# Performance work log

Measured on AMD Instinct MI355X. Metric: run time of the kernel, lower is better.

## Reference

```python
import math
import jax, jax.numpy as jnp
import numpy as np

B, T, D, H, L, DFF = 8, 256, 256, 8, 4, 1024
RBF_DIM = 128
TIME_DIM = D - RBF_DIM  # 128
VOCAB = 64
DH = D // H
RBF_GAP = 0.05
CENTERS = jnp.linspace(0.0, 6.4, RBF_DIM)


def _ln(x, g, b, eps=1e-6):
    m = jnp.mean(x, -1, keepdims=True)
    v = jnp.mean((x - m) ** 2, -1, keepdims=True)
    return (x - m) * jax.lax.rsqrt(v + eps) * g + b


def setup_inputs() -> dict:
    key = jax.random.key(0)
    ks = jax.random.split(key, 24)
    s = 0.02

    def W(k, *shape):
        return jax.random.normal(k, shape, jnp.float32) * s

    emb = W(ks[0], VOCAB, D).at[0].set(0.0)  # padding_idx=0
    return {
        'src': jax.random.randint(ks[1], (B, T), 0, VOCAB),
        'lengths': jax.random.randint(ks[2], (B,), T // 2, T + 1),
        'bond_matrix': jax.random.uniform(ks[3], (B, T, T), jnp.float32, 0.0, 6.4),
        'timestep': jax.random.uniform(ks[4], (B,), jnp.float32, 0.0, 1000.0),
        'emb_table': emb,
        't_w1': W(ks[5], TIME_DIM, TIME_DIM), 't_b1': jnp.zeros((TIME_DIM,), jnp.float32),
        't_w2': W(ks[6], TIME_DIM, TIME_DIM), 't_b2': jnp.zeros((TIME_DIM,), jnp.float32),
        'u': jax.random.normal(ks[7], (D,), jnp.float32) * s,
        'v': jax.random.normal(ks[8], (D,), jnp.float32) * s,
        'Wq': W(ks[9], L, D, D), 'bq': jnp.zeros((L, D), jnp.float32),
        'Wk': W(ks[10], L, D, D), 'bk': jnp.zeros((L, D), jnp.float32),
        'Wv': W(ks[11], L, D, D), 'bv': jnp.zeros((L, D), jnp.float32),
        'Wo': W(ks[12], L, D, D), 'bo': jnp.zeros((L, D), jnp.float32),
        'ln1_g': jnp.ones((L, D), jnp.float32), 'ln1_b': jnp.zeros((L, D), jnp.float32),
        'ln2_g': jnp.ones((L, D), jnp.float32), 'ln2_b': jnp.zeros((L, D), jnp.float32),
        'ff_w1': W(ks[13], L, D, DFF), 'ff_b1': jnp.zeros((L, DFF), jnp.float32),
        'ff_w2': W(ks[14], L, DFF, D), 'ff_b2': jnp.zeros((L, D), jnp.float32),
        'lnf_g': jnp.ones((D,), jnp.float32), 'lnf_b': jnp.zeros((D,), jnp.float32),
    }


def _forward(src, lengths, bond_matrix, timestep, emb_table, t_w1, t_b1, t_w2, t_b2,
             u, v, Wq, bq, Wk, bk, Wv, bv, Wo, bo, ln1_g, ln1_b, ln2_g, ln2_b,
             ff_w1, ff_b1, ff_w2, ff_b2, lnf_g, lnf_b):
    pad = jnp.arange(T) >= lengths[:, None]            # [B,T] True = padding
    pair_mask = pad[:, None, :] | pad[:, :, None]      # [B,T,T]
    # RBF expansion of distances; padded pairs pushed to 1e9 -> rbf ~ 0
    dmat = jnp.where(pair_mask, 1e9, bond_matrix)
    rbf = jnp.exp(-(dmat[..., None] - CENTERS) ** 2 / RBF_GAP)   # [B,T,T,RBF_DIM]
    # sinusoidal timestep embedding -> MLP (Linear, SiLU, Linear)
    half = TIME_DIM // 2
    freqs = jnp.exp(-jnp.log(jnp.asarray(10000.0, jnp.float32)) * jnp.arange(half, dtype=jnp.float32) / half)
    ang = timestep[:, None] * freqs
    temb = jnp.concatenate([jnp.cos(ang), jnp.sin(ang)], -1)
    temb = jax.nn.silu(temb @ t_w1 + t_b1) @ t_w2 + t_b2          # [B,TIME_DIM]
    # pairwise relative embedding: concat(rbf, broadcast time) -> [B,T,T,D]
    rel = jnp.concatenate([rbf, jnp.broadcast_to(temb[:, None, None, :], (B, T, T, TIME_DIM))], -1)
    rel = rel.reshape(B, T, T, H, DH)

    x = emb_table[src]                                  # [B,T,D]
    amask = pad[:, None, None, :]                       # [B,1,1,T]
    uu = u.reshape(H, 1, DH)
    vv = v.reshape(H, 1, DH)
    scale = 1.0 / math.sqrt(DH)

    def step(x, p):
        wq, bq_, wk, bk_, wv, bv_, wo, bo_, g1, b1_, g2, b2_, w1, fb1, w2, fb2 = p
        h = _ln(x, g1, b1_)
        q = (h @ wq + bq_).reshape(B, T, H, DH).transpose(0, 2, 1, 3) * scale
        k = (h @ wk + bk_).reshape(B, T, H, DH).transpose(0, 2, 1, 3)
        val = (h @ wv + bv_).reshape(B, T, H, DH).transpose(0, 2, 1, 3)
        a_c = jnp.einsum('bhqd,bhkd->bhqk', q + uu, k)            # content score
        b_d = jnp.einsum('bhqd,bqkhd->bhqk', q + vv, rel)         # relative-position score
        scores = jnp.where(amask, -1e18, a_c + b_d)
        attn = jax.nn.softmax(scores, -1)
        ctx = jnp.einsum('bhqk,bhkd->bqhd', attn, val).reshape(B, T, D)
        out = ctx @ wo + bo_ + x
        h2 = _ln(out, g2, b2_)
        return jax.nn.relu(h2 @ w1 + fb1) @ w2 + fb2 + out, None

    x, _ = jax.lax.scan(step, x, (Wq, bq, Wk, bk, Wv, bv, Wo, bo,
                                  ln1_g, ln1_b, ln2_g, ln2_b,
                                  ff_w1, ff_b1, ff_w2, ff_b2))
    return _ln(x, lnf_g, lnf_b)


def reference(src, lengths, bond_matrix, timestep, emb_table, t_w1, t_b1, t_w2, t_b2,
              u, v, Wq, bq, Wk, bk, Wv, bv, Wo, bo, ln1_g, ln1_b, ln2_g, ln2_b,
              ff_w1, ff_b1, ff_w2, ff_b2, lnf_g, lnf_b):
    return _forward(src, lengths, bond_matrix, timestep, emb_table, t_w1, t_b1, t_w2, t_b2,
                    u, v, Wq, bq, Wk, bk, Wv, bv, Wo, bo, ln1_g, ln1_b, ln2_g, ln2_b,
                    ff_w1, ff_b1, ff_w2, ff_b2, lnf_g, lnf_b)
```

## Files before the change

kernel.cpp:

```cpp
#include <hip/hip_runtime.h>
#include <hip/hip_bf16.h>
#include <math.h>

#define BB 8
#define TT 256
#define DD 256
#define HH 8
#define DHH 32
#define LL 4
#define DFF 1024
#define QTILE 16

#define RBF_DELTA 0.05039370078740158f
#define RBF_INVGAP 20.0f

typedef __attribute__((ext_vector_type(8))) short short8v;
typedef __attribute__((ext_vector_type(4))) short short4v;
typedef __attribute__((ext_vector_type(4))) float f32x4;

__device__ __forceinline__ ushort f2bf(float x) {
    __hip_bfloat16 h = __float2bfloat16(x);
    return *reinterpret_cast<ushort*>(&h);
}

__global__ void transpose_bf16_kernel(const float* __restrict__ in, ushort* __restrict__ out,
                                      int K, int N, int lstride) {
    __shared__ float tile[32][33];
    int l = blockIdx.z;
    const float* W = in + (size_t)l * lstride;
    ushort* Wt = out + (size_t)l * lstride;
    int kb = blockIdx.y * 32, nb = blockIdx.x * 32;
    int tx = threadIdx.x, ty = threadIdx.y;
#pragma unroll
    for (int i = 0; i < 4; i++) {
        int r = ty + i * 8;
        tile[r][tx] = W[(kb + r) * N + nb + tx];
    }
    __syncthreads();
#pragma unroll
    for (int i = 0; i < 4; i++) {
        int r = ty + i * 8;
        Wt[(nb + r) * K + kb + tx] = f2bf(tile[tx][r]);
    }
}

__global__ void temb_kernel(const float* __restrict__ timestep,
                            const float* __restrict__ t_w1, const float* __restrict__ t_b1,
                            const float* __restrict__ t_w2, const float* __restrict__ t_b2,
                            float* __restrict__ temb_out) {
    __shared__ float s0[128], s1[128];
    int b = blockIdx.x, j = threadIdx.x;
    float ts = timestep[b];
    const float LOG1E4 = 9.210340371976184f;
    if (j < 64) {
        float f = expf(-LOG1E4 * (float)j / 64.f);
        s0[j] = cosf(ts * f);
    } else {
        int i = j - 64;
        float f = expf(-LOG1E4 * (float)i / 64.f);
        s0[j] = sinf(ts * f);
    }
    __syncthreads();
    float acc = t_b1[j];
    for (int i = 0; i < 128; i++) acc += s0[i] * t_w1[i * 128 + j];
    acc = acc / (1.f + expf(-acc));
    s1[j] = acc;
    __syncthreads();
    float acc2 = t_b2[j];
    for (int i = 0; i < 128; i++) acc2 += s1[i] * t_w2[i * 128 + j];
    temb_out[b * 128 + j] = acc2;
}

__global__ void embed_kernel(const int* __restrict__ src, const float* __restrict__ emb,
                             float* __restrict__ x) {
    int r = blockIdx.x, d = threadIdx.x;
    x[r * DD + d] = emb[src[r] * DD + d];
}

template <int OUT_BF16>
__global__ void ln_kernel(const float* __restrict__ in, const float* __restrict__ g,
                          const float* __restrict__ bta, void* __restrict__ out) {
    __shared__ float red[8];
    __shared__ float mv[2];
    int r = blockIdx.x, t = threadIdx.x;
    float v = in[r * DD + t];
    float s = v, s2 = v * v;
    for (int off = 32; off > 0; off >>= 1) {
        s += __shfl_xor(s, off);
        s2 += __shfl_xor(s2, off);
    }
    int w = t >> 6;
    if ((t & 63) == 0) { red[w] = s; red[4 + w] = s2; }
    __syncthreads();
    if (t == 0) {
        float S = red[0] + red[1] + red[2] + red[3];
        float S2 = red[4] + red[5] + red[6] + red[7];
        float m = S * (1.f / 256.f);
        float var = S2 * (1.f / 256.f) - m * m;
        mv[0] = m; mv[1] = rsqrtf(var + 1e-6f);
    }
    __syncthreads();
    float o = (v - mv[0]) * mv[1] * g[t] + bta[t];
    if (OUT_BF16) ((ushort*)out)[r * DD + t] = f2bf(o);
    else          ((float*)out)[r * DD + t] = o;
}

__device__ __forceinline__ void gemm_mfma_body(
    const ushort* __restrict__ A, const ushort* __restrict__ Wt,
    const float* __restrict__ bias, const float* __restrict__ resid,
    void* __restrict__ out, int N, int K, float scale, int RELU, int OUT_BF16) {
    __shared__ __align__(16) ushort smem[10240];
    ushort* As = smem;
    ushort* Bs = smem + 2048;
    float* red = (float*)smem;

    int tid = threadIdx.x;
    int w = tid >> 6, lane = tid & 63;
    int m0 = blockIdx.y * 16, n0 = blockIdx.x * 64;

    f32x4 acc[4] = {f32x4{0,0,0,0}, f32x4{0,0,0,0}, f32x4{0,0,0,0}, f32x4{0,0,0,0}};

    for (int k0 = 0; k0 < K; k0 += 128) {
        {
            int r = tid >> 4, k8 = tid & 15;
            short8v av = *reinterpret_cast<const short8v*>(&A[(m0 + r) * K + k0 + k8 * 8]);
            int dstb = r * 256 + ((k8 * 16) ^ ((r & 7) << 4));
            *reinterpret_cast<short8v*>((char*)As + dstb) = av;
        }
#pragma unroll
        for (int it = 0; it < 4; it++) {
            int idx = it * 256 + tid;
            int r = idx >> 4, k8 = idx & 15;
            short8v bv = *reinterpret_cast<const short8v*>(&Wt[(n0 + r) * K + k0 + k8 * 8]);
            int dstb = r * 256 + ((k8 * 16) ^ ((r & 7) << 4));
            *reinterpret_cast<short8v*>((char*)Bs + dstb) = bv;
        }
        __syncthreads();
        int kb = w * 64 + (lane >> 4) * 16;
        int arow = lane & 15;
        short8v a = *reinterpret_cast<const short8v*>(
            (char*)As + arow * 256 + (kb ^ ((arow & 7) << 4)));
#pragma unroll
        for (int nb = 0; nb < 4; nb++) {
            int nrow = nb * 16 + (lane & 15);
            short8v b = *reinterpret_cast<const short8v*>(
                (char*)Bs + nrow * 256 + (kb ^ ((nrow & 7) << 4)));
            acc[nb] = __builtin_amdgcn_mfma_f32_16x16x32_bf16(a, b, acc[nb], 0, 0, 0);
        }
        __syncthreads();
    }
    if (w > 0) {
        float* r0 = &red[((w - 1) * 64 + lane) * 16];
#pragma unroll
        for (int nb = 0; nb < 4; nb++)
            *reinterpret_cast<f32x4*>(&r0[nb * 4]) = acc[nb];
    }
    __syncthreads();
    if (w == 0) {
        const float* r0 = &red[lane * 16];
        const float* r1 = &red[(64 + lane) * 16];
        const float* r2 = &red[(128 + lane) * 16];
        int col = lane & 15;
#pragma unroll
        for (int nb = 0; nb < 4; nb++) {
            int n = n0 + nb * 16 + col;
            float bia = bias[n];
#pragma unroll
            for (int i = 0; i < 4; i++) {
                int idx = nb * 4 + i;
                int m = m0 + (lane >> 4) * 4 + i;
                float v = acc[nb][i] + r0[idx] + r1[idx] + r2[idx];
                v = (v + bia) * scale;
                if (RELU) v = fmaxf(v, 0.f);
                if (resid) v += resid[m * N + n];
                if (OUT_BF16) ((ushort*)out)[m * N + n] = f2bf(v);
                else          ((float*)out)[m * N + n] = v;
            }
        }
    }
}

template <int RELU, int OUT_BF16>
__global__ __launch_bounds__(256) void gemm_bf16(
    const ushort* __restrict__ A, const ushort* __restrict__ Wt,
    const float* __restrict__ bias, const float* __restrict__ resid,
    void* __restrict__ out, int N, int K, float scale) {
    gemm_mfma_body(A, Wt, bias, resid, out, N, K, scale, RELU, OUT_BF16);
}

__global__ __launch_bounds__(256) void qkv_bf16(
    const ushort* __restrict__ A,
    const ushort* __restrict__ Wqt, const float* __restrict__ bq, float* __restrict__ qo,
    const ushort* __restrict__ Wkt, const float* __restrict__ bk, float* __restrict__ ko,
    const ushort* __restrict__ Wvt, const float* __restrict__ bv, float* __restrict__ vo,
    float qscale) {
    int z = blockIdx.z;
    const ushort* W = (z == 0) ? Wqt : (z == 1) ? Wkt : Wvt;
    const float* bi = (z == 0) ? bq : (z == 1) ? bk : bv;
    float* o = (z == 0) ? qo : (z == 1) ? ko : vo;
    float sc = (z == 0) ? qscale : 1.f;
    gemm_mfma_body(A, W, bi, nullptr, o, DD, DD, sc, 0, 0);
}

__global__ __launch_bounds__(256, 2) void attn_kernel(
    const float* __restrict__ qbuf, const float* __restrict__ kbuf,
    const float* __restrict__ vbuf, const float* __restrict__ u,
    const float* __restrict__ v, const float* __restrict__ temb,
    const float* __restrict__ bond, const int* __restrict__ lengths,
    ushort* __restrict__ ctx) {
    __shared__ float KV[256][33];
    __shared__ float sc[QTILE][257];
    __shared__ float qu_s[QTILE][32], qv_s[QTILE][32];
    __shared__ float tq[QTILE];
    __shared__ float temb_s[32];

    int qt = blockIdx.x;
    int h  = blockIdx.y;
    int b  = blockIdx.z;
    int t  = threadIdx.x;
    int len = lengths[b];
    int q0 = qt * QTILE;

    for (int e = t; e < QTILE * 32; e += 256) {
        int q = e >> 5, dh = e & 31;
        float qs = qbuf[(b * TT + q0 + q) * DD + h * 32 + dh];
        qu_s[q][dh] = qs + u[h * 32 + dh];
        qv_s[q][dh] = qs + v[h * 32 + dh];
    }
    if (t < 32) temb_s[t] = (h >= 4) ? temb[b * 128 + (h - 4) * 32 + t] : 0.f;
    for (int e = t; e < 256 * 32; e += 256) {
        int k = e >> 5, dh = e & 31;
        KV[k][dh] = kbuf[(b * TT + k) * DD + h * 32 + dh];
    }
    __syncthreads();

    if (t < QTILE) {
        float a = 0.f;
#pragma unroll
        for (int j = 0; j < 32; j++) a += qv_s[t][j] * temb_s[j];
        tq[t] = a;
    }
    __syncthreads();

    {
        int k = t;
        bool kvalid = k < len;
        float c0 = (float)(h * 32) * RBF_DELTA;
        for (int q = 0; q < QTILE; q++) {
            float s;
            if (!kvalid) {
                s = -1e18f;
            } else {
                float accA = 0.f;
#pragma unroll
                for (int dh = 0; dh < 32; dh++) accA += qu_s[q][dh] * KV[k][dh];
                float accB;
                if (h < 4) {
                    accB = 0.f;
                    if (q0 + q < len) {
                        float d = bond[(b * TT + q0 + q) * TT + k];
#pragma unroll
                        for (int j = 0; j < 32; j++) {
                            float diff = d - (c0 + j * RBF_DELTA);
                            accB += qv_s[q][j] * __expf(-diff * diff * RBF_INVGAP);
                        }
                    }
                } else {
                    accB = tq[q];
                }
                s = accA + accB;
            }
            sc[q][k] = s;
        }
    }
    __syncthreads();

    {
        int r = t >> 4, j = t & 15;
        float vals[16];
        float mx = -1e30f;
#pragma unroll
        for (int i = 0; i < 16; i++) {
            vals[i] = sc[r][j + 16 * i];
            mx = fmaxf(mx, vals[i]);
        }
        for (int off = 8; off > 0; off >>= 1) mx = fmaxf(mx, __shfl_xor(mx, off));
        float sum = 0.f;
#pragma unroll
        for (int i = 0; i < 16; i++) {
            float e = __expf(vals[i] - mx);
            vals[i] = e; sum += e;
        }
        for (int off = 8; off > 0; off >>= 1) sum += __shfl_xor(sum, off);
        float inv = 1.f / sum;
#pragma unroll
        for (int i = 0; i < 16; i++) sc[r][j + 16 * i] = vals[i] * inv;
    }
    for (int e = t; e < 256 * 32; e += 256) {
        int k2 = e >> 5, dh = e & 31;
        KV[k2][dh] = vbuf[(b * TT + k2) * DD + h * 32 + dh];
    }
    __syncthreads();

    {
        int dh = t & 31, qq = t >> 5;
#pragma unroll
        for (int rep = 0; rep < 2; rep++) {
            int q = qq + 8 * rep;
            float acc = 0.f;
#pragma unroll 8
            for (int k2 = 0; k2 < 256; k2++) acc += sc[q][k2] * KV[k2][dh];
            ctx[(b * TT + q0 + q) * DD + h * 32 + dh] = f2bf(acc);
        }
    }
}

extern "C" void kernel_launch(void* const* d_in, const int* in_sizes, int n_in,
                              void* d_out, int out_size, void* d_ws, size_t ws_size,
                              hipStream_t stream) {
    const int*   src      = (const int*)  d_in[0];
    const int*   lengths  = (const int*)  d_in[1];
    const float* bond     = (const float*)d_in[2];
    const float* timestep = (const float*)d_in[3];
    const float* emb      = (const float*)d_in[4];
    const float* t_w1     = (const float*)d_in[5];
    const float* t_b1     = (const float*)d_in[6];
    const float* t_w2     = (const float*)d_in[7];
    const float* t_b2     = (const float*)d_in[8];
    const float* u        = (const float*)d_in[9];
    const float* v        = (const float*)d_in[10];
    const float* Wq       = (const float*)d_in[11];
    const float* bq       = (const float*)d_in[12];
    const float* Wk       = (const float*)d_in[13];
    const float* bk       = (const float*)d_in[14];
    const float* Wv       = (const float*)d_in[15];
    const float* bv       = (const float*)d_in[16];
    const float* Wo       = (const float*)d_in[17];
    const float* bo       = (const float*)d_in[18];
    const float* ln1_g    = (const float*)d_in[19];
    const float* ln1_b    = (const float*)d_in[20];
    const float* ln2_g    = (const float*)d_in[21];
    const float* ln2_b    = (const float*)d_in[22];
    const float* ff_w1    = (const float*)d_in[23];
    const float* ff_b1    = (const float*)d_in[24];
    const float* ff_w2    = (const float*)d_in[25];
    const float* ff_b2    = (const float*)d_in[26];
    const float* lnf_g    = (const float*)d_in[27];
    const float* lnf_b    = (const float*)d_in[28];

    float* ws   = (float*)d_ws;
    float* xbuf = ws;
    float* qbuf = xbuf + 524288;
    float* kbuf = qbuf + 524288;
    float* vbuf = kbuf + 524288;
    float* obuf = vbuf + 524288;
    float* temb = obuf + 524288;
    ushort* hbuf_bf  = (ushort*)(temb + 1024);
    ushort* cbuf_bf  = hbuf_bf + 524288;
    ushort* ffbuf_bf = cbuf_bf + 524288;
    ushort* wqt_bf   = ffbuf_bf + 2097152;
    ushort* wkt_bf   = wqt_bf + 262144;
    ushort* wvt_bf   = wkt_bf + 262144;
    ushort* wot_bf   = wvt_bf + 262144;
    ushort* ffw1t_bf = wot_bf + 262144;
    ushort* ffw2t_bf = ffw1t_bf + 1048576;

    dim3 tb(32, 8);
    transpose_bf16_kernel<<<dim3(8, 8, 4), tb, 0, stream>>>(Wq, wqt_bf, 256, 256, 65536);
    transpose_bf16_kernel<<<dim3(8, 8, 4), tb, 0, stream>>>(Wk, wkt_bf, 256, 256, 65536);
    transpose_bf16_kernel<<<dim3(8, 8, 4), tb, 0, stream>>>(Wv, wvt_bf, 256, 256, 65536);
    transpose_bf16_kernel<<<dim3(8, 8, 4), tb, 0, stream>>>(Wo, wot_bf, 256, 256, 65536);
    transpose_bf16_kernel<<<dim3(32, 8, 4), tb, 0, stream>>>(ff_w1, ffw1t_bf, 256, 1024, 262144);
    transpose_bf16_kernel<<<dim3(8, 32, 4), tb, 0, stream>>>(ff_w2, ffw2t_bf, 1024, 256, 262144);

    temb_kernel<<<8, 128, 0, stream>>>(timestep, t_w1, t_b1, t_w2, t_b2, temb);
    embed_kernel<<<2048, 256, 0, stream>>>(src, emb, xbuf);

    const float scale = 0.17677669529663687f;
    dim3 gqkv(4, 128, 3);
    dim3 g256(4, 128);
    dim3 g1024(16, 128);

    for (int l = 0; l < LL; l++) {
        ln_kernel<1><<<2048, 256, 0, stream>>>(xbuf, ln1_g + l * 256, ln1_b + l * 256, hbuf_bf);
        qkv_bf16<<<gqkv, 256, 0, stream>>>(hbuf_bf,
            wqt_bf + l * 65536, bq + l * 256, qbuf,
            wkt_bf + l * 65536, bk + l * 256, kbuf,
            wvt_bf + l * 65536, bv + l * 256, vbuf, scale);
        attn_kernel<<<dim3(16, 8, 8), 256, 0, stream>>>(qbuf, kbuf, vbuf, u, v, temb, bond, lengths, cbuf_bf);
        gemm_bf16<0, 0><<<g256, 256, 0, stream>>>(cbuf_bf, wot_bf + l * 65536, bo + l * 256, xbuf, obuf, 256, 256, 1.f);
        ln_kernel<1><<<2048, 256, 0, stream>>>(obuf, ln2_g + l * 256, ln2_b + l * 256, hbuf_bf);
        gemm_bf16<1, 1><<<g1024, 256, 0, stream>>>(hbuf_bf, ffw1t_bf + l * 262144, ff_b1 + l * 1024, nullptr, ffbuf_bf, 1024, 256, 1.f);
        gemm_bf16<0, 0><<<g256, 256, 0, stream>>>(ffbuf_bf, ffw2t_bf + l * 262144, ff_b2 + l * 256, obuf, xbuf, 256, 1024, 1.f);
    }
    ln_kernel<0><<<2048, 256, 0, stream>>>(xbuf, lnf_g, lnf_b, (float*)d_out);
}
```

Measured before the change: 606.2 us.

## Restructure attention kernel: swizzled K/V smem, K in registers, vectorized loads, exp2 RBF

Replaces the padded K/V shared-memory tiles with an XOR-swizzled layout and caches each thread's key row in registers, so the score loop reads q through broadcast float4 loads. The RBF term now uses exp2f with a prefolded constant and an incremental diff instead of recomputing each centre. The score row stride is padded to 260 so float4 reads of the score tile are aligned, and launch bounds request 3 blocks per CU. The cost is more register pressure from the 32-float key cache alongside a higher occupancy target, which could cause spills.

```diff
diff --git a/kernel.cpp b/kernel.cpp
--- a/kernel.cpp
+++ b/kernel.cpp
@@ -12,7 +12,7 @@
 #define QTILE 16
 
 #define RBF_DELTA 0.05039370078740158f
-#define RBF_INVGAP 20.0f
+#define RBF_NEGK -28.853900817779268f
 
 typedef __attribute__((ext_vector_type(8))) short short8v;
 typedef __attribute__((ext_vector_type(4))) short short4v;
@@ -202,14 +202,14 @@
     gemm_mfma_body(A, W, bi, nullptr, o, DD, DD, sc, 0, 0);
 }
 
-__global__ __launch_bounds__(256, 2) void attn_kernel(
+__global__ __launch_bounds__(256, 3) void attn_kernel(
     const float* __restrict__ qbuf, const float* __restrict__ kbuf,
     const float* __restrict__ vbuf, const float* __restrict__ u,
     const float* __restrict__ v, const float* __restrict__ temb,
     const float* __restrict__ bond, const int* __restrict__ lengths,
     ushort* __restrict__ ctx) {
-    __shared__ float KV[256][33];
-    __shared__ float sc[QTILE][257];
+    __shared__ float KV[256 * 32];
+    __shared__ float sc[QTILE][260];
     __shared__ float qu_s[QTILE][32], qv_s[QTILE][32];
     __shared__ float tq[QTILE];
     __shared__ float temb_s[32];
@@ -230,7 +230,7 @@
     if (t < 32) temb_s[t] = (h >= 4) ? temb[b * 128 + (h - 4) * 32 + t] : 0.f;
     for (int e = t; e < 256 * 32; e += 256) {
         int k = e >> 5, dh = e & 31;
-        KV[k][dh] = kbuf[(b * TT + k) * DD + h * 32 + dh];
+        KV[k * 32 + (dh ^ (k & 31))] = kbuf[(b * TT + k) * DD + h * 32 + dh];
     }
     __syncthreads();
 
@@ -241,6 +241,13 @@
         tq[t] = a;
     }
     __syncthreads();
+
+    float kreg[32];
+    {
+        int kx = t & 31;
+#pragma unroll
+        for (int dh = 0; dh < 32; dh++) kreg[dh] = KV[t * 32 + (dh ^ kx)];
+    }
 
     {
         int k = t;
@@ -251,18 +258,35 @@
             if (!kvalid) {
                 s = -1e18f;
             } else {
+                const float* qur = qu_s[q];
                 float accA = 0.f;
 #pragma unroll
-                for (int dh = 0; dh < 32; dh++) accA += qu_s[q][dh] * KV[k][dh];
+                for (int c = 0; c < 8; c++) {
+                    float4 q4 = *reinterpret_cast<const float4*>(&qur[c * 4]);
+                    accA = fmaf(q4.x, kreg[c * 4 + 0], accA);
+                    accA = fmaf(q4.y, kreg[c * 4 + 1], accA);
+                    accA = fmaf(q4.z, kreg[c * 4 + 2], accA);
+                    accA = fmaf(q4.w, kreg[c * 4 + 3], accA);
+                }
                 float accB;
                 if (h < 4) {
                     accB = 0.f;
                     if (q0 + q < len) {
-                        float d = bond[(b * TT + q0 + q) * TT + k];
-#pragma unroll
-                        for (int j = 0; j < 32; j++) {
-                            float diff = d - (c0 + j * RBF_DELTA);
-                            accB += qv_s[q][j] * __expf(-diff * diff * RBF_INVGAP);
+                        float d = bond[(size_t)(b * TT + q0 + q) * TT + k];
+                        float diff = d - c0;
+                        const float* qvr = qv_s[q];
+#pragma unroll
+                        for (int c = 0; c < 8; c++) {
+                            float4 q4 = *reinterpret_cast<const float4*>(&qvr[c * 4]);
+                            float p;
+                            p = exp2f(diff * diff * RBF_NEGK);
+                            accB = fmaf(q4.x, p, accB); diff -= RBF_DELTA;
+                            p = exp2f(diff * diff * RBF_NEGK);
+                            accB = fmaf(q4.y, p, accB); diff -= RBF_DELTA;
+                            p = exp2f(diff * diff * RBF_NEGK);
+                            accB = fmaf(q4.z, p, accB); diff -= RBF_DELTA;
+                            p = exp2f(diff * diff * RBF_NEGK);
+                            accB = fmaf(q4.w, p, accB); diff -= RBF_DELTA;
                         }
                     }
                 } else {
@@ -270,7 +294,7 @@
                 }
                 s = accA + accB;
             }
-            sc[q][k] = s;
+            sc[q][t] = s;
         }
     }
     __syncthreads();
@@ -298,7 +322,7 @@
     }
     for (int e = t; e < 256 * 32; e += 256) {
         int k2 = e >> 5, dh = e & 31;
-        KV[k2][dh] = vbuf[(b * TT + k2) * DD + h * 32 + dh];
+        KV[k2 * 32 + (dh ^ (k2 & 31))] = vbuf[(b * TT + k2) * DD + h * 32 + dh];
     }
     __syncthreads();
 
@@ -309,7 +333,13 @@
             int q = qq + 8 * rep;
             float acc = 0.f;
 #pragma unroll 8
-            for (int k2 = 0; k2 < 256; k2++) acc += sc[q][k2] * KV[k2][dh];
+            for (int kk = 0; kk < 256; kk += 4) {
+                float4 s4 = *reinterpret_cast<const float4*>(&sc[q][kk]);
+                acc = fmaf(s4.x, KV[(kk + 0) * 32 + (dh ^ ((kk + 0) & 31))], acc);
+                acc = fmaf(s4.y, KV[(kk + 1) * 32 + (dh ^ ((kk + 1) & 31))], acc);
+                acc = fmaf(s4.z, KV[(kk + 2) * 32 + (dh ^ ((kk + 2) & 31))], acc);
+                acc = fmaf(s4.w, KV[(kk + 3) * 32 + (dh ^ ((kk + 3) & 31))], acc);
+            }
             ctx[(b * TT + q0 + q) * DD + h * 32 + dh] = f2bf(acc);
         }
     }
```

Measured after the change: 580.4 us. 1.04x faster.
